# Kernel tuning notes

Hardware: AMD Instinct MI355X
Metric: run time of the kernel (lower is better)

Reference implementation:

```python
import jax, jax.numpy as jnp
import numpy as np

N, E = 100000, 1600000
D_IN, D_HID, D_OUT = 128, 64, 64
NEG_SLOPE = 0.2


def setup_inputs() -> dict:
    key = jax.random.key(0)
    ks = jax.random.split(key, 12)
    x = jax.random.normal(ks[0], (N, D_IN), dtype=jnp.float32)
    edge_index = jax.random.randint(ks[1], (2, E), 0, N, dtype=jnp.int64)
    edge_attr = jax.random.normal(ks[2], (E, 8), dtype=jnp.float32)
    s1 = 1.0 / np.sqrt(D_IN)
    s2 = 1.0 / np.sqrt(D_HID)
    return {
        "x": x,
        "edge_index": edge_index,
        "edge_attr": edge_attr,
        "W1": jax.random.normal(ks[3], (D_IN, D_HID), dtype=jnp.float32) * s1,
        "att_src1": jax.random.normal(ks[4], (D_HID,), dtype=jnp.float32) * s2,
        "att_dst1": jax.random.normal(ks[5], (D_HID,), dtype=jnp.float32) * s2,
        "b1": jnp.zeros((D_HID,), dtype=jnp.float32),
        "W2": jax.random.normal(ks[6], (D_HID, D_OUT), dtype=jnp.float32) * s2,
        "att_src2": jax.random.normal(ks[7], (D_OUT,), dtype=jnp.float32) * (1.0 / np.sqrt(D_OUT)),
        "att_dst2": jax.random.normal(ks[8], (D_OUT,), dtype=jnp.float32) * (1.0 / np.sqrt(D_OUT)),
        "b2": jnp.zeros((D_OUT,), dtype=jnp.float32),
    }


def gat_conv(x, src, dst, W, att_src, att_dst, b, n_nodes):
    # h = W x  (single head)
    h = x @ W                                   # [N, F]
    a_src = h @ att_src                         # [N]
    a_dst = h @ att_dst                         # [N]
    e = jax.nn.leaky_relu(a_src[src] + a_dst[dst], NEG_SLOPE)  # [E]
    # softmax over incoming edges per target node (numerically stable)
    e_max = jax.ops.segment_max(e, dst, num_segments=n_nodes)
    w = jnp.exp(e - e_max[dst])
    denom = jax.ops.segment_sum(w, dst, num_segments=n_nodes)
    alpha = w / (denom[dst] + 1e-16)            # [E]
    out = jax.ops.segment_sum(h[src] * alpha[:, None], dst, num_segments=n_nodes)
    return out + b


def reference(x, edge_index, edge_attr, W1, att_src1, att_dst1, b1, W2, att_src2, att_dst2, b2):
    n_nodes = x.shape[0]
    # PyG GATConv default: add self-loops; edge_attr unused (edge_dim=None)
    loops = jnp.arange(n_nodes, dtype=edge_index.dtype)
    src = jnp.concatenate([edge_index[0], loops])
    dst = jnp.concatenate([edge_index[1], loops])
    h = gat_conv(x, src, dst, W1, att_src1, att_dst1, b1, n_nodes)
    h = jax.nn.relu(h)
    h = gat_conv(h, src, dst, W2, att_src2, att_dst2, b2, n_nodes)
    # global_mean_pool with batch=None -> mean over all nodes, shape [1, D_OUT]
    return jnp.mean(h, axis=0, keepdims=True)
```

## Files before the change

### kernel.cpp

```cpp
#include <hip/hip_runtime.h>
#include <hip/hip_bf16.h>
#include <cstdint>

#define NEG_SLOPE 0.2f
#define SCAN_ELEMS 1024
#define BUCKET_SHIFT 9
#define CHUNK 8192

typedef __attribute__((ext_vector_type(4))) int            i32x4;
typedef __attribute__((ext_vector_type(4))) float          f32x4;
typedef __attribute__((ext_vector_type(8))) unsigned short u16x8;

__device__ inline unsigned short f2bf(float f) {
    unsigned xi = __float_as_uint(f);
    unsigned r = xi + 0x7fffu + ((xi >> 16) & 1u);
    return (unsigned short)(r >> 16);
}
__device__ inline float bflo(unsigned g) { return __uint_as_float((g & 0xffffu) << 16); }
__device__ inline float bfhi(unsigned g) { return __uint_as_float(g & 0xffff0000u); }

__device__ inline int get_ei(const int* ei, int is64, long idx) {
    return is64 ? ei[2 * idx] : ei[(int)idx];
}

__device__ inline int detect_is64(const int* __restrict__ ei, int tid) {
    __shared__ int dred[4];
    int v = 0;
    for (int i = tid; i < 2048; i += 256) v |= ei[2 * i + 1];
#pragma unroll
    for (int off = 32; off; off >>= 1) v |= __shfl_xor(v, off);
    if ((tid & 63) == 0) dred[tid >> 6] = v;
    __syncthreads();
    int r = dred[0] | dred[1] | dred[2] | dred[3];
    __syncthreads();
    return (r == 0) ? 1 : 0;
}

__global__ __launch_bounds__(256) void p1_hist(const int* __restrict__ ei,
                                               int* __restrict__ HH,
                                               int E, int n, int nblk) {
    __shared__ int cnt[256];
    int tid = threadIdx.x;
    int is64 = detect_is64(ei, tid);
    int nbuk = (n + (1 << BUCKET_SHIFT) - 1) >> BUCKET_SHIFT;
    for (int b = tid; b < nbuk; b += 256) cnt[b] = 0;
    __syncthreads();
    int total = E + n;
    int beg = blockIdx.x * CHUNK;
    int end = beg + CHUNK; if (end > total) end = total;
    for (int i = beg + tid; i < end; i += 256) {
        int d = (i < E) ? get_ei(ei, is64, (long)E + i) : (i - E);
        atomicAdd(&cnt[d >> BUCKET_SHIFT], 1);
    }
    __syncthreads();
    for (int b = tid; b < nbuk; b += 256) HH[b * nblk + blockIdx.x] = cnt[b];
}

__global__ __launch_bounds__(256) void scan1_kernel(const int* __restrict__ src,
                                                    int* __restrict__ bsums, int n) {
    int t = threadIdx.x;
    int i0 = blockIdx.x * SCAN_ELEMS + 4 * t;
    int4 v = make_int4(0, 0, 0, 0);
    if (i0 + 3 < n) v = *(const int4*)(src + i0);
    else {
        if (i0 + 0 < n) v.x = src[i0 + 0];
        if (i0 + 1 < n) v.y = src[i0 + 1];
        if (i0 + 2 < n) v.z = src[i0 + 2];
        if (i0 + 3 < n) v.w = src[i0 + 3];
    }
    int s = v.x + v.y + v.z + v.w;
#pragma unroll
    for (int off = 32; off; off >>= 1) s += __shfl_down(s, off);
    __shared__ int ws[4];
    if ((t & 63) == 0) ws[t >> 6] = s;
    __syncthreads();
    if (t == 0) bsums[blockIdx.x] = ws[0] + ws[1] + ws[2] + ws[3];
}

__global__ __launch_bounds__(256) void scan3g_kernel(const int* __restrict__ src,
                                                     const int* __restrict__ bsums,
                                                     int* __restrict__ out, int n, int nb) {
    int b = blockIdx.x;
    int t = threadIdx.x;
    __shared__ int sb[256];
    int bv = (t < nb) ? bsums[t] : 0;
    sb[t] = bv;
    __syncthreads();
    for (int off = 1; off < 256; off <<= 1) {
        int u = (t >= off) ? sb[t - off] : 0;
        __syncthreads();
        sb[t] += u;
        __syncthreads();
    }
    int blockbase = (b == 0) ? 0 : sb[b - 1];

    int i0 = b * SCAN_ELEMS + 4 * t;
    int4 v = make_int4(0, 0, 0, 0);
    if (i0 + 3 < n) v = *(const int4*)(src + i0);
    else {
        if (i0 + 0 < n) v.x = src[i0 + 0];
        if (i0 + 1 < n) v.y = src[i0 + 1];
        if (i0 + 2 < n) v.z = src[i0 + 2];
        if (i0 + 3 < n) v.w = src[i0 + 3];
    }
    int s0 = v.x, s1 = s0 + v.y, s2 = s1 + v.z, s3 = s2 + v.w;
    __shared__ int sh[256];
    sh[t] = s3;
    __syncthreads();
    for (int off = 1; off < 256; off <<= 1) {
        int u = (t >= off) ? sh[t - off] : 0;
        __syncthreads();
        sh[t] += u;
        __syncthreads();
    }
    int base = blockbase + sh[t] - s3;
    if (i0 + 0 < n) out[i0 + 0] = base;
    if (i0 + 1 < n) out[i0 + 1] = base + s0;
    if (i0 + 2 < n) out[i0 + 2] = base + s1;
    if (i0 + 3 < n) out[i0 + 3] = base + s2;
}

__global__ __launch_bounds__(256) void p3_scatter(const int* __restrict__ ei,
                                                  const int* __restrict__ scanHH,
                                                  int* __restrict__ sorted,
                                                  int E, int n, int nblk) {
    __shared__ int base[256];
    __shared__ int cur[256];
    int tid = threadIdx.x;
    int is64 = detect_is64(ei, tid);
    int nbuk = (n + (1 << BUCKET_SHIFT) - 1) >> BUCKET_SHIFT;
    for (int b = tid; b < nbuk; b += 256) {
        base[b] = scanHH[b * nblk + blockIdx.x];
        cur[b] = 0;
    }
    __syncthreads();
    int total = E + n;
    int beg = blockIdx.x * CHUNK;
    int end = beg + CHUNK; if (end > total) end = total;
    for (int i = beg + tid; i < end; i += 256) {
        int s, d;
        if (i < E) {
            s = get_ei(ei, is64, i);
            d = get_ei(ei, is64, (long)E + i);
        } else {
            s = d = i - E;
        }
        int b = d >> BUCKET_SHIFT;
        int p = base[b] + atomicAdd(&cur[b], 1);
        sorted[p] = (s << BUCKET_SHIFT) | (d & ((1 << BUCKET_SHIFT) - 1));
    }
}

__global__ __launch_bounds__(256) void p4_finalize(const int* __restrict__ scanHH,
                                                   const int* __restrict__ sorted,
                                                   int* __restrict__ ptr,
                                                   int* __restrict__ csr_src,
                                                   int n, int nblk, int T) {
    int b = blockIdx.x;
    int nbuk = gridDim.x;
    int tid = threadIdx.x;
    int node0 = b << BUCKET_SHIFT;
    int nn = n - node0; if (nn > (1 << BUCKET_SHIFT)) nn = 1 << BUCKET_SHIFT;
    int beg = scanHH[b * nblk];
    int end = (b + 1 < nbuk) ? scanHH[(b + 1) * nblk] : T;

    __shared__ int cnt[512];
    __shared__ int pair[256];
    __shared__ int exc[512];
    cnt[tid] = 0; cnt[tid + 256] = 0;
    __syncthreads();
    for (int j = beg + tid; j < end; j += 256) {
        int v = sorted[j];
        atomicAdd(&cnt[v & ((1 << BUCKET_SHIFT) - 1)], 1);
    }
    __syncthreads();
    int psum = cnt[2 * tid] + cnt[2 * tid + 1];
    pair[tid] = psum;
    __syncthreads();
    for (int off = 1; off < 256; off <<= 1) {
        int u = (tid >= off) ? pair[tid - off] : 0;
        __syncthreads();
        pair[tid] += u;
        __syncthreads();
    }
    int pexc = pair[tid] - psum;
    exc[2 * tid] = pexc;
    exc[2 * tid + 1] = pexc + cnt[2 * tid];
    __syncthreads();
    for (int i = tid; i < nn; i += 256) ptr[node0 + i] = beg + exc[i];
    if (node0 + nn == n && tid == 0) ptr[n] = T;
    cnt[tid] = exc[tid]; cnt[tid + 256] = exc[tid + 256];
    __syncthreads();
    for (int j = beg + tid; j < end; j += 256) {
        int v = sorted[j];
        int p = beg + atomicAdd(&cnt[v & ((1 << BUCKET_SHIFT) - 1)], 1);
        csr_src[p] = ((unsigned)v) >> BUCKET_SHIFT;
    }
}

__global__ __launch_bounds__(256) void pack_w(const float* __restrict__ W1,
                                              const float* __restrict__ W2,
                                              unsigned short* __restrict__ wp1,
                                              unsigned short* __restrict__ wp2) {
    int t = blockIdx.x * 256 + threadIdx.x;
    if (t >= 24 * 64) return;
    int f = t >> 6, l = t & 63;
    int lm = l & 15, lg = l >> 4;
    const float* W = (f < 16) ? W1 : W2;
    unsigned short* wp = (f < 16) ? wp1 : wp2;
    int idx = (f < 16) ? f : (f - 16);
    int kt = idx >> 2, ct = idx & 3;
    union { u16x8 v; unsigned short u[8]; } o;
#pragma unroll
    for (int e = 0; e < 8; ++e)
        o.u[e] = f2bf(W[(size_t)(32 * kt + 8 * lg + e) * 64 + 16 * ct + lm]);
    *(u16x8*)(wp + ((size_t)idx * 64 + l) * 8) = o.v;
}

#define MFMA_BF16(acc, a, b) \
    asm("s_nop 1\n\tv_mfma_f32_16x16x32_bf16 %0, %1, %2, %0" \
        : "+v"(acc) : "v"(a), "v"(b))

template <int KT>
__global__ __launch_bounds__(256) void proj_mfma(const float* __restrict__ x,
                                                 const unsigned short* __restrict__ Wp,
                                                 const float* __restrict__ att_s,
                                                 const float* __restrict__ att_d,
                                                 unsigned short* __restrict__ h2,
                                                 float* __restrict__ asrc,
                                                 float* __restrict__ adst, int n) {
    constexpr int K = 32 * KT;
    __shared__ alignas(16) unsigned short lb[4][16 * 72];
    int tid = threadIdx.x;
    int wid = tid >> 6, l = tid & 63;
    int lm = l & 15, lg = l >> 4;

    int node0 = blockIdx.x * 64 + wid * 16;
    if (node0 >= n) return;

    float as_c[4], ad_c[4];
#pragma unroll
    for (int ct = 0; ct < 4; ++ct) {
        as_c[ct] = att_s[16 * ct + lm];
        ad_c[ct] = att_d[16 * ct + lm];
    }

    f32x4 acc[4] = {};

    int arow = node0 + lm;
    bool rowok = arow < n;
    const float* xp = x + (size_t)arow * K + 8 * lg;

#pragma unroll
    for (int kt = 0; kt < KT; ++kt) {
        float4 v0 = make_float4(0.f, 0.f, 0.f, 0.f);
        float4 v1 = v0;
        if (rowok) {
            v0 = *(const float4*)(xp + 32 * kt);
            v1 = *(const float4*)(xp + 32 * kt + 4);
        }
        i32x4 af;
        af[0] = (int)((unsigned)f2bf(v0.x) | ((unsigned)f2bf(v0.y) << 16));
        af[1] = (int)((unsigned)f2bf(v0.z) | ((unsigned)f2bf(v0.w) << 16));
        af[2] = (int)((unsigned)f2bf(v1.x) | ((unsigned)f2bf(v1.y) << 16));
        af[3] = (int)((unsigned)f2bf(v1.z) | ((unsigned)f2bf(v1.w) << 16));
#pragma unroll
        for (int ct = 0; ct < 4; ++ct) {
            i32x4 bf = *(const i32x4*)(Wp + (((kt * 4 + ct) * 64) + l) * 8);
            MFMA_BF16(acc[ct], af, bf);
        }
    }
    asm volatile("s_nop 7\n\ts_nop 7"
                 : "+v"(acc[0]), "+v"(acc[1]), "+v"(acc[2]), "+v"(acc[3]));

    float ps[4], pd[4];
#pragma unroll
    for (int r = 0; r < 4; ++r) {
        float s = 0.f, d = 0.f;
#pragma unroll
        for (int ct = 0; ct < 4; ++ct) {
            s = fmaf(acc[ct][r], as_c[ct], s);
            d = fmaf(acc[ct][r], ad_c[ct], d);
        }
        ps[r] = s; pd[r] = d;
    }
#pragma unroll
    for (int off = 1; off < 16; off <<= 1) {
#pragma unroll
        for (int r = 0; r < 4; ++r) {
            ps[r] += __shfl_xor(ps[r], off);
            pd[r] += __shfl_xor(pd[r], off);
        }
    }
    if (lm == 0) {
#pragma unroll
        for (int r = 0; r < 4; ++r) {
            int node = node0 + 4 * lg + r;
            if (node < n) { asrc[node] = ps[r]; adst[node] = pd[r]; }
        }
    }

    unsigned short* wb = lb[wid];
#pragma unroll
    for (int ct = 0; ct < 4; ++ct)
#pragma unroll
        for (int r = 0; r < 4; ++r)
            wb[(4 * lg + r) * 72 + 16 * ct + lm] = f2bf(acc[ct][r]);
    asm volatile("s_waitcnt lgkmcnt(0)" ::: "memory");
    int ch = l & 7;
#pragma unroll
    for (int p = 0; p < 2; ++p) {
        int rr = (l >> 3) + 8 * p;
        u16x8 ov = *(const u16x8*)(wb + rr * 72 + 8 * ch);
        int onode = node0 + rr;
        if (onode < n)
            *(u16x8*)(h2 + (size_t)onode * 64 + 8 * ch) = ov;
    }
}

template <bool FMEAN>
__global__ __launch_bounds__(256) void agg_kernel(const int* __restrict__ ptr,
                                                  const int* __restrict__ srcs,
                                                  const unsigned short* __restrict__ h2,
                                                  const float* __restrict__ asrc,
                                                  const float* __restrict__ adst,
                                                  const float* __restrict__ bias,
                                                  float* __restrict__ outrow,
                                                  float* __restrict__ partials,
                                                  int n, int do_relu) {
    __shared__ int   sm_s[4][64];
    __shared__ float sm_w[4][64];
    __shared__ float red[256];
    int tid = threadIdx.x;
    int lane = tid & 63, wid = tid >> 6;
    int half = lane >> 5, fp = lane & 31;
    const char* h2b = (const char*)h2;
    unsigned fpo = (unsigned)fp << 2;
    float b0 = bias[2 * fp], b1 = bias[2 * fp + 1];
    float msum0 = 0.f, msum1 = 0.f;

    int gwave = (blockIdx.x * blockDim.x + tid) >> 6;
    int nwaves = (gridDim.x * blockDim.x) >> 6;
    for (int node = gwave; node < n; node += nwaves) {
        int beg = ptr[node], end = ptr[node + 1];
        float ad = adst[node];
        float acc0 = 0.f, acc1 = 0.f, wsum = 0.f;
        for (int b = beg; b < end; b += 64) {
            int blen = end - b; if (blen > 64) blen = 64;
            int sv = 0; float wv = 0.f;
            if (lane < blen) {
                sv = srcs[b + lane];
                float e = asrc[sv] + ad;
                e = (e > 0.f) ? e : NEG_SLOPE * e;
                wv = __expf(e);
            }
            wsum += wv;
            sm_s[wid][lane] = sv;
            sm_w[wid][lane] = wv;
            int np4 = ((((blen + 1) >> 1) + 3) >> 2);
            for (int j4 = 0; j4 < np4; ++j4) {
                int jb = 4 * j4;
                int ss[4]; float ww[4]; unsigned gg[4];
#pragma unroll
                for (int u = 0; u < 4; ++u) {
                    int e0 = 2 * (jb + u) + half;
                    ss[u] = sm_s[wid][e0];
                    ww[u] = sm_w[wid][e0];
                }
#pragma unroll
                for (int u = 0; u < 4; ++u)
                    gg[u] = *(const unsigned*)(h2b + (((unsigned)ss[u] << 7) + fpo));
#pragma unroll
                for (int u = 0; u < 4; ++u) {
                    acc0 = fmaf(ww[u], bflo(gg[u]), acc0);
                    acc1 = fmaf(ww[u], bfhi(gg[u]), acc1);
                }
            }
        }
        acc0 += __shfl_xor(acc0, 32);
        acc1 += __shfl_xor(acc1, 32);
#pragma unroll
        for (int off = 32; off; off >>= 1) wsum += __shfl_xor(wsum, off);
        float inv = 1.f / (wsum + 1e-16f);
        float o0 = acc0 * inv + b0;
        float o1 = acc1 * inv + b1;
        if (!FMEAN) {
            if (do_relu) { o0 = fmaxf(o0, 0.f); o1 = fmaxf(o1, 0.f); }
            if (half == 0)
                *(float2*)(outrow + (size_t)node * 64 + 2 * fp) = make_float2(o0, o1);
        } else {
            if (half == 0) { msum0 += o0; msum1 += o1; }
        }
    }
    if (FMEAN) {
        if (half == 0) {
            red[wid * 64 + 2 * fp] = msum0;
            red[wid * 64 + 2 * fp + 1] = msum1;
        }
        __syncthreads();
        if (tid < 64) {
            float t = red[tid] + red[64 + tid] + red[128 + tid] + red[192 + tid];
            partials[(size_t)blockIdx.x * 64 + tid] = t;
        }
    }
}

__global__ __launch_bounds__(256) void reduce_mean(const float* __restrict__ partials,
                                                   float* __restrict__ out,
                                                   int nb, float inv_n) {
    __shared__ float red[256];
    int f = threadIdx.x & 63;
    int w = threadIdx.x >> 6;
    int idx = blockIdx.x * 4 + w;
    int stride = gridDim.x * 4;
    float s = 0.f;
    for (int r = idx; r < nb; r += stride) s += partials[(size_t)r * 64 + f];
    red[threadIdx.x] = s;
    __syncthreads();
    if (w == 0) {
        float t = red[f] + red[64 + f] + red[128 + f] + red[192 + f];
        atomicAdd(&out[f], t * inv_n);
    }
}

extern "C" void kernel_launch(void* const* d_in, const int* in_sizes, int n_in,
                              void* d_out, int out_size, void* d_ws, size_t ws_size,
                              hipStream_t stream) {
    const float* x   = (const float*)d_in[0];
    const int*   ei  = (const int*)d_in[1];
    const float* W1  = (const float*)d_in[3];
    const float* as1 = (const float*)d_in[4];
    const float* ad1 = (const float*)d_in[5];
    const float* b1  = (const float*)d_in[6];
    const float* W2  = (const float*)d_in[7];
    const float* as2 = (const float*)d_in[8];
    const float* ad2 = (const float*)d_in[9];
    const float* b2  = (const float*)d_in[10];
    float* out = (float*)d_out;

    const int N = in_sizes[0] / 128;
    const int E = in_sizes[1] / 2;
    const int T = E + N;

    const int NBUK = (N + (1 << BUCKET_SHIFT) - 1) >> BUCKET_SHIFT;
    const int NBLK = (T + CHUNK - 1) / CHUNK;
    const int NHH  = NBUK * NBLK;
    const int NBS  = (NHH + SCAN_ELEMS - 1) / SCAN_ELEMS;
    const int AGRID = (N + 3) / 4;

    size_t off = 0;
    char* base = (char*)d_ws;
    auto alloc = [&](size_t bytes) -> void* {
        void* p = base + off;
        off += (bytes + 255) & ~(size_t)255;
        return p;
    };
    int*   ptr     = (int*)alloc(((size_t)N + 1) * 4);
    int*   bsums   = (int*)alloc(256 * 4);
    int*   HH      = (int*)alloc((size_t)NHH * 4);
    int*   scanHH  = (int*)alloc((size_t)NHH * 4);
    int*   csr_src = (int*)alloc((size_t)T * 4);
    float* asrc    = (float*)alloc((size_t)N * 4);
    float* adst    = (float*)alloc((size_t)N * 4);
    unsigned short* h2 = (unsigned short*)alloc((size_t)N * 64 * 2);
    float* bufB    = (float*)alloc((size_t)N * 64 * 4);
    unsigned short* wp1 = (unsigned short*)alloc(16 * 64 * 8 * 2);
    unsigned short* wp2 = (unsigned short*)alloc(8 * 64 * 8 * 2);
    int*   sorted  = (int*)bufB;
    float* partials = bufB;
    (void)ws_size;

    pack_w<<<6, 256, 0, stream>>>(W1, W2, wp1, wp2);

    p1_hist<<<NBLK, 256, 0, stream>>>(ei, HH, E, N, NBLK);
    scan1_kernel<<<NBS, 256, 0, stream>>>(HH, bsums, NHH);
    scan3g_kernel<<<NBS, 256, 0, stream>>>(HH, bsums, scanHH, NHH, NBS);
    p3_scatter<<<NBLK, 256, 0, stream>>>(ei, scanHH, sorted, E, N, NBLK);
    p4_finalize<<<NBUK, 256, 0, stream>>>(scanHH, sorted, ptr, csr_src, N, NBLK, T);

    const int PGRID = (N + 63) / 64;

    proj_mfma<4><<<PGRID, 256, 0, stream>>>(x, wp1, as1, ad1, h2, asrc, adst, N);
    agg_kernel<false><<<AGRID, 256, 0, stream>>>(ptr, csr_src, h2, asrc, adst,
                                                 b1, bufB, nullptr, N, 1);

    proj_mfma<2><<<PGRID, 256, 0, stream>>>(bufB, wp2, as2, ad2, h2, asrc, adst, N);
    agg_kernel<true><<<AGRID, 256, 0, stream>>>(ptr, csr_src, h2, asrc, adst,
                                                b2, nullptr, partials, N, 0);
    hipMemsetAsync(out, 0, 64 * 4, stream);
    reduce_mean<<<64, 256, 0, stream>>>(partials, out, AGRID, 1.f / (float)N);
}
```

Measured before the change: 342.1 us.

## Store layer-1 activations as bf16 and gather 8-byte rows per lane in aggregation

The first aggregation now writes its ReLU output directly as bf16 instead of fp32, and the second projection reads that bf16 tensor straight into MFMA operands, skipping the conversion. This halves the intermediate write and read traffic. The aggregation kernel is also restructured so each lane gathers 4 features (8 bytes) of one of 4 edges at a time rather than 2 features of 2 edges, with source index and weight packed together in shared memory. This trades more shuffle reductions per node for fewer, wider gathers, and rounding the activation to bf16 earlier is an equivalent quantisation point since the projection already converted it.

```diff
diff --git a/kernel.cpp b/kernel.cpp
--- a/kernel.cpp
+++ b/kernel.cpp
@@ -10,13 +10,14 @@
 typedef __attribute__((ext_vector_type(4))) int            i32x4;
 typedef __attribute__((ext_vector_type(4))) float          f32x4;
 typedef __attribute__((ext_vector_type(8))) unsigned short u16x8;
+typedef __attribute__((ext_vector_type(4))) unsigned short u16x4;
 
 __device__ inline unsigned short f2bf(float f) {
     unsigned xi = __float_as_uint(f);
     unsigned r = xi + 0x7fffu + ((xi >> 16) & 1u);
     return (unsigned short)(r >> 16);
 }
-__device__ inline float bflo(unsigned g) { return __uint_as_float((g & 0xffffu) << 16); }
+__device__ inline float bflo(unsigned g) { return __uint_as_float(g << 16); }
 __device__ inline float bfhi(unsigned g) { return __uint_as_float(g & 0xffff0000u); }
 
 __device__ inline int get_ei(const int* ei, int is64, long idx) {
@@ -221,8 +222,8 @@
     asm("s_nop 1\n\tv_mfma_f32_16x16x32_bf16 %0, %1, %2, %0" \
         : "+v"(acc) : "v"(a), "v"(b))
 
-template <int KT>
-__global__ __launch_bounds__(256) void proj_mfma(const float* __restrict__ x,
+template <int KT, bool XBF>
+__global__ __launch_bounds__(256) void proj_mfma(const void* __restrict__ xin,
                                                  const unsigned short* __restrict__ Wp,
                                                  const float* __restrict__ att_s,
                                                  const float* __restrict__ att_d,
@@ -249,21 +250,27 @@
 
     int arow = node0 + lm;
     bool rowok = arow < n;
-    const float* xp = x + (size_t)arow * K + 8 * lg;
 
 #pragma unroll
     for (int kt = 0; kt < KT; ++kt) {
-        float4 v0 = make_float4(0.f, 0.f, 0.f, 0.f);
-        float4 v1 = v0;
-        if (rowok) {
-            v0 = *(const float4*)(xp + 32 * kt);
-            v1 = *(const float4*)(xp + 32 * kt + 4);
-        }
-        i32x4 af;
-        af[0] = (int)((unsigned)f2bf(v0.x) | ((unsigned)f2bf(v0.y) << 16));
-        af[1] = (int)((unsigned)f2bf(v0.z) | ((unsigned)f2bf(v0.w) << 16));
-        af[2] = (int)((unsigned)f2bf(v1.x) | ((unsigned)f2bf(v1.y) << 16));
-        af[3] = (int)((unsigned)f2bf(v1.z) | ((unsigned)f2bf(v1.w) << 16));
+        i32x4 af = {0, 0, 0, 0};
+        if (XBF) {
+            const unsigned short* xb = (const unsigned short*)xin
+                                       + (size_t)arow * K + 32 * kt + 8 * lg;
+            if (rowok) af = *(const i32x4*)xb;
+        } else {
+            const float* xp = (const float*)xin + (size_t)arow * K + 8 * lg + 32 * kt;
+            float4 v0 = make_float4(0.f, 0.f, 0.f, 0.f);
+            float4 v1 = v0;
+            if (rowok) {
+                v0 = *(const float4*)(xp);
+                v1 = *(const float4*)(xp + 4);
+            }
+            af[0] = (int)((unsigned)f2bf(v0.x) | ((unsigned)f2bf(v0.y) << 16));
+            af[1] = (int)((unsigned)f2bf(v0.z) | ((unsigned)f2bf(v0.w) << 16));
+            af[2] = (int)((unsigned)f2bf(v1.x) | ((unsigned)f2bf(v1.y) << 16));
+            af[3] = (int)((unsigned)f2bf(v1.z) | ((unsigned)f2bf(v1.w) << 16));
+        }
 #pragma unroll
         for (int ct = 0; ct < 4; ++ct) {
             i32x4 bf = *(const i32x4*)(Wp + (((kt * 4 + ct) * 64) + l) * 8);
@@ -325,26 +332,25 @@
                                                   const float* __restrict__ asrc,
                                                   const float* __restrict__ adst,
                                                   const float* __restrict__ bias,
-                                                  float* __restrict__ outrow,
+                                                  unsigned short* __restrict__ outbf,
                                                   float* __restrict__ partials,
                                                   int n, int do_relu) {
-    __shared__ int   sm_s[4][64];
-    __shared__ float sm_w[4][64];
+    __shared__ int2  sm[4][64];
     __shared__ float red[256];
     int tid = threadIdx.x;
     int lane = tid & 63, wid = tid >> 6;
-    int half = lane >> 5, fp = lane & 31;
+    int slot = lane >> 4, f = lane & 15;
     const char* h2b = (const char*)h2;
-    unsigned fpo = (unsigned)fp << 2;
-    float b0 = bias[2 * fp], b1 = bias[2 * fp + 1];
-    float msum0 = 0.f, msum1 = 0.f;
+    unsigned fo = (unsigned)f << 3;
+    float4 bv = *(const float4*)(bias + 4 * f);
+    float ms0 = 0.f, ms1 = 0.f, ms2 = 0.f, ms3 = 0.f;
 
     int gwave = (blockIdx.x * blockDim.x + tid) >> 6;
     int nwaves = (gridDim.x * blockDim.x) >> 6;
     for (int node = gwave; node < n; node += nwaves) {
         int beg = ptr[node], end = ptr[node + 1];
         float ad = adst[node];
-        float acc0 = 0.f, acc1 = 0.f, wsum = 0.f;
+        float a0 = 0.f, a1 = 0.f, a2 = 0.f, a3 = 0.f, wsum = 0.f;
         for (int b = beg; b < end; b += 64) {
             int blen = end - b; if (blen > 64) blen = 64;
             int sv = 0; float wv = 0.f;
@@ -355,48 +361,51 @@
                 wv = __expf(e);
             }
             wsum += wv;
-            sm_s[wid][lane] = sv;
-            sm_w[wid][lane] = wv;
-            int np4 = ((((blen + 1) >> 1) + 3) >> 2);
-            for (int j4 = 0; j4 < np4; ++j4) {
-                int jb = 4 * j4;
-                int ss[4]; float ww[4]; unsigned gg[4];
-#pragma unroll
-                for (int u = 0; u < 4; ++u) {
-                    int e0 = 2 * (jb + u) + half;
-                    ss[u] = sm_s[wid][e0];
-                    ww[u] = sm_w[wid][e0];
-                }
-#pragma unroll
-                for (int u = 0; u < 4; ++u)
-                    gg[u] = *(const unsigned*)(h2b + (((unsigned)ss[u] << 7) + fpo));
-#pragma unroll
-                for (int u = 0; u < 4; ++u) {
-                    acc0 = fmaf(ww[u], bflo(gg[u]), acc0);
-                    acc1 = fmaf(ww[u], bfhi(gg[u]), acc1);
+            sm[wid][lane] = make_int2(sv, __float_as_int(wv));
+            int ni = (blen + 7) >> 3;
+            for (int j = 0; j < ni; ++j) {
+#pragma unroll
+                for (int u = 0; u < 2; ++u) {
+                    int e0 = 8 * j + 4 * u + slot;
+                    int2 swp = sm[wid][e0];
+                    float w = __int_as_float(swp.y);
+                    uint2 g = *(const uint2*)(h2b + (((unsigned)swp.x << 7) + fo));
+                    a0 = fmaf(w, bflo(g.x), a0);
+                    a1 = fmaf(w, bfhi(g.x), a1);
+                    a2 = fmaf(w, bflo(g.y), a2);
+                    a3 = fmaf(w, bfhi(g.y), a3);
                 }
             }
         }
-        acc0 += __shfl_xor(acc0, 32);
-        acc1 += __shfl_xor(acc1, 32);
+        a0 += __shfl_xor(a0, 16); a0 += __shfl_xor(a0, 32);
+        a1 += __shfl_xor(a1, 16); a1 += __shfl_xor(a1, 32);
+        a2 += __shfl_xor(a2, 16); a2 += __shfl_xor(a2, 32);
+        a3 += __shfl_xor(a3, 16); a3 += __shfl_xor(a3, 32);
 #pragma unroll
         for (int off = 32; off; off >>= 1) wsum += __shfl_xor(wsum, off);
         float inv = 1.f / (wsum + 1e-16f);
-        float o0 = acc0 * inv + b0;
-        float o1 = acc1 * inv + b1;
+        float o0 = a0 * inv + bv.x;
+        float o1 = a1 * inv + bv.y;
+        float o2 = a2 * inv + bv.z;
+        float o3 = a3 * inv + bv.w;
         if (!FMEAN) {
-            if (do_relu) { o0 = fmaxf(o0, 0.f); o1 = fmaxf(o1, 0.f); }
-            if (half == 0)
-                *(float2*)(outrow + (size_t)node * 64 + 2 * fp) = make_float2(o0, o1);
+            if (do_relu) {
+                o0 = fmaxf(o0, 0.f); o1 = fmaxf(o1, 0.f);
+                o2 = fmaxf(o2, 0.f); o3 = fmaxf(o3, 0.f);
+            }
+            if (slot == 0) {
+                u16x4 ov;
+                ov[0] = f2bf(o0); ov[1] = f2bf(o1);
+                ov[2] = f2bf(o2); ov[3] = f2bf(o3);
+                *(u16x4*)(outbf + (size_t)node * 64 + 4 * f) = ov;
+            }
         } else {
-            if (half == 0) { msum0 += o0; msum1 += o1; }
+            if (slot == 0) { ms0 += o0; ms1 += o1; ms2 += o2; ms3 += o3; }
         }
     }
     if (FMEAN) {
-        if (half == 0) {
-            red[wid * 64 + 2 * fp] = msum0;
-            red[wid * 64 + 2 * fp + 1] = msum1;
-        }
+        if (slot == 0)
+            *(float4*)(red + wid * 64 + 4 * f) = make_float4(ms0, ms1, ms2, ms3);
         __syncthreads();
         if (tid < 64) {
             float t = red[tid] + red[64 + tid] + red[128 + tid] + red[192 + tid];
@@ -463,11 +472,11 @@
     float* asrc    = (float*)alloc((size_t)N * 4);
     float* adst    = (float*)alloc((size_t)N * 4);
     unsigned short* h2 = (unsigned short*)alloc((size_t)N * 64 * 2);
-    float* bufB    = (float*)alloc((size_t)N * 64 * 4);
+    unsigned short* bufB = (unsigned short*)alloc((size_t)N * 64 * 4);
     unsigned short* wp1 = (unsigned short*)alloc(16 * 64 * 8 * 2);
     unsigned short* wp2 = (unsigned short*)alloc(8 * 64 * 8 * 2);
     int*   sorted  = (int*)bufB;
-    float* partials = bufB;
+    float* partials = (float*)bufB;
     (void)ws_size;
 
     pack_w<<<6, 256, 0, stream>>>(W1, W2, wp1, wp2);
@@ -480,11 +489,11 @@
 
     const int PGRID = (N + 63) / 64;
 
-    proj_mfma<4><<<PGRID, 256, 0, stream>>>(x, wp1, as1, ad1, h2, asrc, adst, N);
+    proj_mfma<4, false><<<PGRID, 256, 0, stream>>>(x, wp1, as1, ad1, h2, asrc, adst, N);
     agg_kernel<false><<<AGRID, 256, 0, stream>>>(ptr, csr_src, h2, asrc, adst,
                                                  b1, bufB, nullptr, N, 1);
 
-    proj_mfma<2><<<PGRID, 256, 0, stream>>>(bufB, wp2, as2, ad2, h2, asrc, adst, N);
+    proj_mfma<2, true><<<PGRID, 256, 0, stream>>>(bufB, wp2, as2, ad2, h2, asrc, adst, N);
     agg_kernel<true><<<AGRID, 256, 0, stream>>>(ptr, csr_src, h2, asrc, adst,
                                                 b2, nullptr, partials, N, 0);
     hipMemsetAsync(out, 0, 64 * 4, stream);
```

Result: no change. 346.0 us (+1.1%).
